# Kernel tuning notes

Measured on AMD Instinct MI355X. Metric: run time of the kernel, lower is better.

Reference implementation:

```python
import jax, jax.numpy as jnp
import numpy as np

H = 488          # hardcoded grid size in the module
K = 6            # n_targets
ITERS = 10       # n_iterations
RADIUS = 2       # sample_radius (int, used in slicing)
RECLEN = 2 * RADIUS + 1   # avgpool kernel in TorchModalitySampler (upscale=1)
RES = 0.25
THR = 3.0 / RES  # mask threshold on distances


def _greedy_sample(hm):
    """TorchModalitySampler greedy peak extraction for one [H,H] heatmap."""
    aw = H - RECLEN + 1  # avgpool output size (stride 1, valid)

    def step(hm, _):
        # avgpool(kernel=RECLEN, stride=1)
        agg = jax.lax.reduce_window(hm, 0.0, jax.lax.add,
                                    (RECLEN, RECLEN), (1, 1), 'VALID') / (RECLEN * RECLEN)
        flat = jnp.argmax(agg)              # first occurrence of max (row-major)
        r, c = flat // aw, flat % aw
        win = jax.lax.dynamic_slice(hm, (r, c), (RECLEN, RECLEN))
        max_val = win.max()
        # torch.nonzero(hm == max_val)[0] == first row-major match
        fh = jnp.argmax(hm == max_val)
        pt = jnp.stack([fh // H, fh % H]).astype(jnp.float32)
        conf = win.sum()
        hm = jax.lax.dynamic_update_slice(hm, jnp.zeros((RECLEN, RECLEN), hm.dtype), (r, c))
        return hm, (pt, conf)

    _, (pts, confs) = jax.lax.scan(step, hm, None, length=K)
    return pts, confs  # [K,2] float, [K] float


def setup_inputs() -> dict:
    key = jax.random.key(0)
    heatmap = jax.random.uniform(key, (32, 1, H, H), dtype=jnp.float32)
    return {"heatmap": heatmap}


def reference(heatmap):
    B = heatmap.shape[0]
    hm2d = heatmap[:, 0]                       # [B,H,H]
    clusters, _pre_conf = jax.vmap(_greedy_sample)(hm2d)   # [B,K,2]

    ii, jj = jnp.meshgrid(jnp.arange(H), jnp.arange(H), indexing='ij')
    indices = jnp.stack([ii, jj], -1).reshape(-1, 2).astype(jnp.float32)  # [N,2]
    hm_flat = hm2d.reshape(B, -1)              # [B,N]

    def body(_, cl):
        # d: [B,K,N] distances from each cluster to every pixel
        d = jnp.maximum(jnp.linalg.norm(indices[None, None] - cl[:, :, None], axis=-1), 0.001)
        m = d.min(axis=1)                      # [B,N] nearest-cluster distance
        w = (d < THR) * (hm_flat[:, None] / d) * (m[:, None] / d)  # [B,K,N]
        return jnp.einsum('bkn,nd->bkd', w, indices) / w.sum(-1, keepdims=True)

    clusters = jax.lax.fori_loop(0, ITERS, body, clusters)
    new_clusters = jnp.round(clusters).astype(jnp.int32)   # [B,K,2]

    def conf_one(hm, c):
        win = jax.lax.dynamic_slice(hm, (c[0] - RADIUS, c[1] - RADIUS), (2 * RADIUS, 2 * RADIUS))
        return win.sum()

    confidences = jax.vmap(lambda hm, cs: jax.vmap(lambda c: conf_one(hm, c))(cs))(hm2d, new_clusters)
    return new_clusters, confidences
```

## Files before the change

### kernel.cpp

```cpp
#include <hip/hip_runtime.h>

#define H   488
#define HH  (H*H)
#define AW  484
#define KK  6
#define BB  32
#define NB4 (HH/4)
#define NCH 10
#define MAGIC 0x137F9E24

#define SCALE 8388608.0f

#define PHYS(j) ((j) + ((j) >> 5))
#define HPAD 504

__device__ __forceinline__ float mload(const float* h, int i, int j,
                                       const int* rr, const int* rc, int nr) {
    float v = h[i * H + j];
    for (int t = 0; t < nr; ++t)
        if ((unsigned)(i - rr[t]) < 5u && (unsigned)(j - rc[t]) < 5u) v = 0.0f;
    return v;
}

__device__ __forceinline__ unsigned long long mkkey(int s, int c) {
    return ((unsigned long long)(unsigned)s << 32) | (unsigned)~(unsigned)c;
}

union SmAB {
    int colsum[8][HPAD];
    struct { unsigned long long bK[8 * AW]; unsigned long long rvK[AW]; } kb;
};

__global__ __launch_bounds__(640) void kAB(const float* __restrict__ hm,
                                           unsigned long long* __restrict__ blockK,
                                           int* __restrict__ rectR, int* __restrict__ rectC,
                                           float* __restrict__ maxv, int* __restrict__ scanres,
                                           int* __restrict__ doneA, int* __restrict__ cntC) {
    __shared__ SmAB sm;
    __shared__ int rrS[KK], rcS[KK];
    __shared__ int selRs, selCs;
    int tid = threadIdx.x, wave = tid >> 6, lane = tid & 63;

    if (blockIdx.x >= 32) {
        int idx = blockIdx.x - 32;
        int b  = idx / 61;
        int g  = idx - b * 61;
        int r0 = g * 8;
        int nw = (r0 + 8 <= AW) ? 8 : (AW - r0);
        const float* h = hm + b * HH;

        int j = tid;
        if (j < H) {
            int v[12];
            #pragma unroll
            for (int i = 0; i < 12; ++i) {
                int row = r0 + i;
                v[i] = (row < H) ? (int)(h[row * H + j] * SCALE) : 0;
            }
            int pj = PHYS(j);
            #pragma unroll
            for (int w = 0; w < 8; ++w)
                sm.colsum[w][pj] = v[w] + v[w + 1] + v[w + 2] + v[w + 3] + v[w + 4];
        }
        __syncthreads();

        if (wave < nw) {
            int r = r0 + wave;
            int c0 = lane * 8;
            int cs[13];
            #pragma unroll
            for (int t = 0; t < 13; ++t) {
                int ix = c0 + t;
                cs[t] = (ix < H) ? sm.colsum[wave][PHYS(ix)] : 0;
            }
            int s = cs[0] + cs[1] + cs[2] + cs[3] + cs[4];
            unsigned long long best = (c0 < AW) ? mkkey(s, c0) : 0ull;
            #pragma unroll
            for (int t = 1; t < 8; ++t) {
                s += cs[t + 4] - cs[t - 1];
                int c = c0 + t;
                unsigned long long k2v = (c < AW) ? mkkey(s, c) : 0ull;
                if (k2v > best) best = k2v;
            }
            #pragma unroll
            for (int off = 4; off; off >>= 1) {
                unsigned long long o = __shfl_down(best, (unsigned)off);
                if (o > best) best = o;
            }
            if ((lane & 7) == 0) {
                int p = lane >> 3;
                __hip_atomic_store(&blockK[(b * 8 + p) * AW + r], best,
                                   __ATOMIC_RELAXED, __HIP_MEMORY_SCOPE_AGENT);
            }
        }
        __syncthreads();
        if (tid == 0)
            __hip_atomic_store(&doneA[b * 61 + g], MAGIC,
                               __ATOMIC_RELAXED, __HIP_MEMORY_SCOPE_AGENT);
        return;
    }

    int b = blockIdx.x;
    const float* h = hm + b * HH;

    if (tid == 0) cntC[b] = 0;

    if (wave == 0) {
        bool done = false;
        do {
            int v = (lane < 61)
                ? __hip_atomic_load(&doneA[b * 61 + lane], __ATOMIC_RELAXED, __HIP_MEMORY_SCOPE_AGENT)
                : MAGIC;
            done = __all(v == MAGIC);
            if (!done) __builtin_amdgcn_s_sleep(8);
        } while (!done);
        __threadfence();
    }
    __syncthreads();

    if (tid < AW) {
        unsigned long long kk[8];
        #pragma unroll
        for (int p = 0; p < 8; ++p) kk[p] = blockK[(b * 8 + p) * AW + tid];
        unsigned long long mk = kk[0];
        #pragma unroll
        for (int p = 1; p < 8; ++p) if (kk[p] > mk) mk = kk[p];
        #pragma unroll
        for (int p = 0; p < 8; ++p) sm.kb.bK[p * AW + tid] = kk[p];
        sm.kb.rvK[tid] = ((mk >> 32) << 20) | ((unsigned long long)(1023 - tid) << 10) | (mk & 0x3FF);
    }
    __syncthreads();

    unsigned long long partK = 0ull;
    int prlo = 0, prhi = -1;

    for (int step = 0; step < KK; ++step) {
        if (wave == 0) {
            unsigned long long win = 0ull;
            if (step == 0) {
                #pragma unroll
                for (int t = 0; t < 8; ++t) {
                    int idx = t * 64 + lane;
                    if (idx < AW) { unsigned long long v = sm.kb.rvK[idx]; if (v > win) win = v; }
                }
                #pragma unroll
                for (int off = 32; off; off >>= 1) {
                    unsigned long long o = __shfl_down(win, (unsigned)off);
                    if (o > win) win = o;
                }
            } else {
                if (lane <= prhi - prlo) win = sm.kb.rvK[prlo + lane];
                if (lane == 9) { if (partK > win) win = partK; }
                #pragma unroll
                for (int off = 8; off; off >>= 1) {
                    unsigned long long o = __shfl_down(win, (unsigned)off);
                    if (o > win) win = o;
                }
            }
            if (lane == 0) {
                int C = 1023 - (int)(win & 0x3FF);
                int R = 1023 - (int)((win >> 10) & 0x3FF);
                rrS[step] = R; rcS[step] = C;
                selRs = R; selCs = C;
            }
        } else if (wave == 1 && step > 0) {
            int m = step - 1;
            int R1 = rrS[m], C1 = rcS[m];
            float wv = -1.0f;
            if (lane < 25) wv = mload(h, R1 + lane / 5, C1 + lane % 5, rrS, rcS, m);
            #pragma unroll
            for (int off = 32; off; off >>= 1) wv = fmaxf(wv, __shfl_down(wv, (unsigned)off));
            if (lane == 0) {
                maxv[b * KK + m]    = wv;
                rectR[b * KK + m]   = R1;
                rectC[b * KK + m]   = C1;
                scanres[b * KK + m] = 0x7fffffff;
            }
        }
        __syncthreads();
        if (step == KK - 1) break;

        int R = selRs, C = selCs;
        int rlo = R > 4 ? R - 4 : 0, rhi = R + 4 < AW ? R + 4 : AW - 1;
        int nr = rhi - rlo + 1;
        if (wave >= 1 && wave <= nr) {
            int r = rlo + (wave - 1);
            int cb0 = (C > 4 ? C - 4 : 0) >> 6;
            int cb1 = ((C + 4 < AW ? C + 4 : AW - 1)) >> 6;
            bool two = (cb1 > cb0);
            int rrL[KK], rcL[KK];
            #pragma unroll
            for (int t = 0; t < KK; ++t) { rrL[t] = rrS[t]; rcL[t] = rcS[t]; }
            int jA0 = cb0 * 64 + lane, jB0 = jA0 + 64;
            int jA1 = cb1 * 64 + lane, jB1 = jA1 + 64;
            float vA0[5], vB0[5], vA1[5], vB1[5];
            #pragma unroll
            for (int i = 0; i < 5; ++i) {
                vA0[i] = (jA0 < H) ? h[(r + i) * H + jA0] : 0.0f;
                vB0[i] = (lane < 4 && jB0 < H) ? h[(r + i) * H + jB0] : 0.0f;
                vA1[i] = (two && jA1 < H) ? h[(r + i) * H + jA1] : 0.0f;
                vB1[i] = (two && lane < 4 && jB1 < H) ? h[(r + i) * H + jB1] : 0.0f;
            }
            #pragma unroll
            for (int t = 0; t < KK; ++t) if (t <= step) {
                int rt = rrL[t], ct = rcL[t];
                #pragma unroll
                for (int i = 0; i < 5; ++i) {
                    if ((unsigned)(r + i - rt) < 5u) {
                        if ((unsigned)(jA0 - ct) < 5u) vA0[i] = 0.0f;
                        if ((unsigned)(jB0 - ct) < 5u) vB0[i] = 0.0f;
                        if ((unsigned)(jA1 - ct) < 5u) vA1[i] = 0.0f;
                        if ((unsigned)(jB1 - ct) < 5u) vB1[i] = 0.0f;
                    }
                }
            }
            int csA0 = 0, csB0 = 0, csA1 = 0, csB1 = 0;
            #pragma unroll
            for (int i = 0; i < 5; ++i) {
                csA0 += (int)(vA0[i] * SCALE); csB0 += (int)(vB0[i] * SCALE);
                csA1 += (int)(vA1[i] * SCALE); csB1 += (int)(vB1[i] * SCALE);
            }
            int s0 = 0, s1 = 0;
            #pragma unroll
            for (int k = 0; k < 5; ++k) {
                int a0 = __shfl_down(csA0, (unsigned)k);
                int a1 = __shfl_down(csA1, (unsigned)k);
                int srcb = lane + k - 64; if (srcb < 0) srcb = 0;
                int b0v = __shfl(csB0, srcb);
                int b1v = __shfl(csB1, srcb);
                s0 += (lane + k < 64) ? a0 : b0v;
                s1 += (lane + k < 64) ? a1 : b1v;
            }
            int c0col = cb0 * 64 + lane, c1col = cb1 * 64 + lane;
            unsigned long long kA_ = (c0col < AW) ? mkkey(s0, c0col) : 0ull;
            unsigned long long kB_ = (two && c1col < AW) ? mkkey(s1, c1col) : 0ull;
            #pragma unroll
            for (int off = 32; off; off >>= 1) {
                unsigned long long oA = __shfl_down(kA_, (unsigned)off);
                unsigned long long oB = __shfl_down(kB_, (unsigned)off);
                if (oA > kA_) kA_ = oA;
                if (oB > kB_) kB_ = oB;
            }
            unsigned long long keyA = __shfl(kA_, 0);
            unsigned long long keyB = __shfl(kB_, 0);
            unsigned long long cand = (lane < 8) ? sm.kb.bK[lane * AW + r] : 0ull;
            if (lane == cb0) cand = keyA;
            if (two && lane == cb1) cand = keyB;
            #pragma unroll
            for (int off = 4; off; off >>= 1) {
                unsigned long long o = __shfl_down(cand, (unsigned)off);
                if (o > cand) cand = o;
            }
            if (lane == 0) {
                sm.kb.rvK[r] = ((cand >> 32) << 20) | ((unsigned long long)(1023 - r) << 10) | (cand & 0x3FF);
                sm.kb.bK[cb0 * AW + r] = keyA;
                if (two) sm.kb.bK[cb1 * AW + r] = keyB;
            }
        } else if (wave == 0) {
            unsigned long long c0 = 0ull;
            #pragma unroll
            for (int t = 0; t < 8; ++t) {
                int idx = t * 64 + lane;
                if (idx < AW && (idx < rlo || idx > rhi)) {
                    unsigned long long v = sm.kb.rvK[idx];
                    if (v > c0) c0 = v;
                }
            }
            #pragma unroll
            for (int off = 32; off; off >>= 1) {
                unsigned long long o = __shfl_down(c0, (unsigned)off);
                if (o > c0) c0 = o;
            }
            partK = __shfl(c0, 0);
            prlo = rlo; prhi = rhi;
        }
        __syncthreads();
    }
    if (wave == 1) {
        int m = KK - 1;
        int R1 = rrS[m], C1 = rcS[m];
        float wv = -1.0f;
        if (lane < 25) wv = mload(h, R1 + lane / 5, C1 + lane % 5, rrS, rcS, m);
        #pragma unroll
        for (int off = 32; off; off >>= 1) wv = fmaxf(wv, __shfl_down(wv, (unsigned)off));
        if (lane == 0) {
            maxv[b * KK + m]    = wv;
            rectR[b * KK + m]   = R1;
            rectC[b * KK + m]   = C1;
            scanres[b * KK + m] = 0x7fffffff;
        }
    }
}

__global__ __launch_bounds__(768) void kCD(const float* __restrict__ hm,
                                           const int* __restrict__ rectR, const int* __restrict__ rectC,
                                           const float* __restrict__ maxv, int* __restrict__ scanres,
                                           int* __restrict__ cntC, float* __restrict__ out) {
    int b     = blockIdx.x & 31;
    int chunk = blockIdx.x >> 5;
    int tid = threadIdx.x, wave = tid >> 6, lane = tid & 63;
    const float* h = hm + b * HH;

    {
        float mv[KK];
        int rr[5], rc[5], lim[KK];
        #pragma unroll
        for (int s = 0; s < KK; ++s) mv[s] = maxv[b * KK + s];
        float minmv = mv[0];
        #pragma unroll
        for (int s = 1; s < KK; ++s) minmv = fminf(minmv, mv[s]);
        #pragma unroll
        for (int t = 0; t < 5; ++t) { rr[t] = rectR[b * KK + t]; rc[t] = rectC[b * KK + t]; }
        int limmax = 0;
        #pragma unroll
        for (int s = 0; s < KK; ++s) {
            lim[s] = (rectR[b * KK + s] + 4) * H + rectC[b * KK + s] + 4;
            limmax = lim[s] > limmax ? lim[s] : limmax;
        }
        const float4* h4 = (const float4*)h;
        int local[KK];
        #pragma unroll
        for (int s = 0; s < KK; ++s) local[s] = 0x7fffffff;
        for (int i4 = chunk * 768 + tid; i4 < NB4; i4 += 768 * NCH) {
            if (4 * i4 > limmax) break;
            float4 v = h4[i4];
            float m4 = fmaxf(fmaxf(v.x, v.y), fmaxf(v.z, v.w));
            if (m4 >= minmv) {
                float vs[4] = {v.x, v.y, v.z, v.w};
                #pragma unroll
                for (int e = 0; e < 4; ++e) {
                    #pragma unroll
                    for (int s = 0; s < KK; ++s) {
                        if (vs[e] == mv[s]) {
                            int n = 4 * i4 + e;
                            if (n <= lim[s]) {
                                int i = n / H, j = n - i * H;
                                bool masked = false;
                                for (int t = 0; t < s; ++t)
                                    if ((unsigned)(i - rr[t]) < 5u && (unsigned)(j - rc[t]) < 5u) masked = true;
                                if (!masked && n < local[s]) local[s] = n;
                            }
                        }
                    }
                }
            }
        }
        __shared__ int smC[KK];
        if (tid < KK) smC[tid] = 0x7fffffff;
        __syncthreads();
        #pragma unroll
        for (int s = 0; s < KK; ++s)
            if (local[s] != 0x7fffffff) atomicMin(&smC[s], local[s]);
        __syncthreads();
        if (tid < KK && smC[tid] != 0x7fffffff)
            atomicMin(&scanres[b * KK + tid], smC[tid]);
    }
    __syncthreads();

    __shared__ int sh_old;
    if (tid == 0) sh_old = atomicAdd(&cntC[b], 1);
    __syncthreads();
    if (sh_old != NCH - 1) return;

    __shared__ float cly[2][KK], clx[2][KK];
    __shared__ float part[KK][2][3];
    if (tid < KK) {
        int fh = atomicMin(&scanres[b * KK + tid], 0x7fffffff);
        cly[0][tid] = (float)(fh / H);
        clx[0][tid] = (float)(fh % H);
    }
    __syncthreads();
    int k = wave >> 1, half = wave & 1;
    int base = half * 64 + lane;

    int di_[4], dj_[4]; bool act_[4];
    #pragma unroll
    for (int s = 0; s < 4; ++s) { act_[s] = false; di_[s] = 0; dj_[s] = 0; }
    {
        int pos = 0;
        #pragma unroll
        for (int r = 0; r < 24; ++r) {
            const int di = r - 11;
            const int u = (di > 0) ? (di - 1) : -di;
            const int vt[12] = {11, 11, 11, 11, 11, 10, 10, 9, 8, 7, 6, 4};
            const int vl = vt[u];
            const int cnt = 2 * vl + 2;
            #pragma unroll
            for (int s = 0; s < 4; ++s) {
                int idx = base + s * 128;
                if (idx >= pos && idx < pos + cnt) {
                    act_[s] = true; di_[s] = di; dj_[s] = -vl + (idx - pos);
                }
            }
            pos += cnt;
        }
    }

    int cur = 0;
    for (int it = 0; it < 10; ++it) {
        float ys[KK], xs[KK];
        #pragma unroll
        for (int q = 0; q < KK; ++q) { ys[q] = cly[cur][q]; xs[q] = clx[cur][q]; }
        float cy = 0.0f, cx = 0.0f;
        #pragma unroll
        for (int q = 0; q < KK; ++q) if (q == k) { cy = ys[q]; cx = xs[q]; }
        int fy = (int)floorf(cy), fx = (int)floorf(cx);
        float sy = 0.0f, sx = 0.0f, sw = 0.0f;
        #pragma unroll
        for (int s = 0; s < 4; ++s) {
            if (act_[s]) {
                int i = fy + di_[s], j = fx + dj_[s];
                if ((unsigned)i < (unsigned)H && (unsigned)j < (unsigned)H) {
                    float hv = h[i * H + j];
                    float fi = (float)i, fj = (float)j;
                    float d2[KK];
                    #pragma unroll
                    for (int q = 0; q < KK; ++q) {
                        float dy = __fsub_rn(fi, ys[q]);
                        float dx = __fsub_rn(fj, xs[q]);
                        d2[q] = __fadd_rn(__fmul_rn(dy, dy), __fmul_rn(dx, dx));
                    }
                    float dyk = __fsub_rn(fi, cy), dxk = __fsub_rn(fj, cx);
                    float d2k = __fadd_rn(__fmul_rn(dyk, dyk), __fmul_rn(dxk, dxk));
                    if (d2k < 144.0f) {
                        float m2 = d2[0];
                        #pragma unroll
                        for (int q = 1; q < KK; ++q) m2 = fminf(m2, d2[q]);
                        float d = fmaxf(__fsqrt_rn(d2k), 0.001f);
                        float m = fmaxf(__fsqrt_rn(m2), 0.001f);
                        float w = __fmul_rn(__fdiv_rn(hv, d), __fdiv_rn(m, d));
                        sw += w;
                        sy += w * fi;
                        sx += w * fj;
                    }
                }
            }
        }
        #pragma unroll
        for (int off = 32; off; off >>= 1) {
            sy += __shfl_down(sy, (unsigned)off);
            sx += __shfl_down(sx, (unsigned)off);
            sw += __shfl_down(sw, (unsigned)off);
        }
        if (lane == 0) { part[k][half][0] = sy; part[k][half][1] = sx; part[k][half][2] = sw; }
        __syncthreads();
        if (tid < KK) {
            float ty = part[tid][0][0] + part[tid][1][0];
            float tx = part[tid][0][1] + part[tid][1][1];
            float tw = part[tid][0][2] + part[tid][1][2];
            cly[cur ^ 1][tid] = ty / tw;
            clx[cur ^ 1][tid] = tx / tw;
        }
        __syncthreads();
        cur ^= 1;
    }
    if (tid < KK) {
        int iy = __float2int_rn(cly[cur][tid]);
        int ix = __float2int_rn(clx[cur][tid]);
        out[b * (KK * 2) + 2 * tid]     = (float)iy;
        out[b * (KK * 2) + 2 * tid + 1] = (float)ix;
        int s0 = iy - 2; if (s0 < 0) s0 = 0; if (s0 > H - 4) s0 = H - 4;
        int s1 = ix - 2; if (s1 < 0) s1 = 0; if (s1 > H - 4) s1 = H - 4;
        double cs = 0.0;
        for (int i = 0; i < 4; ++i)
            for (int j = 0; j < 4; ++j) cs += (double)h[(s0 + i) * H + (s1 + j)];
        out[BB * KK * 2 + b * KK + tid] = (float)cs;
    }
}

extern "C" void kernel_launch(void* const* d_in, const int* in_sizes, int n_in,
                              void* d_out, int out_size, void* d_ws, size_t ws_size,
                              hipStream_t stream) {
    const float* hm = (const float*)d_in[0];
    float* out = (float*)d_out;

    unsigned long long* blockK = (unsigned long long*)d_ws;
    int*    rectR   = (int*)(blockK + BB * 8 * AW);
    int*    rectC   = rectR + BB * KK;
    float*  maxv    = (float*)(rectC + BB * KK);
    int*    scanres = (int*)(maxv + BB * KK);
    int*    cntC    = scanres + BB * KK;
    int*    doneA   = cntC + BB;

    kAB<<<32 + BB * 61, 640, 0, stream>>>(hm, blockK, rectR, rectC, maxv, scanres, doneA, cntC);
    kCD<<<BB * NCH, 768, 0, stream>>>(hm, rectR, rectC, maxv, scanres, cntC, out);
}
```

Measured before the change: 146.7 us.

## Replace spin-waiting reducer blocks with last-arriving-block finalization

Removes the 32 dedicated blocks that spin on completion flags. Each of the row-group blocks now publishes its flag, checks whether all 61 flags for its batch are set, and the block that sees completion runs the greedy selection tail. The goal is to stop wasting CU slots on spin loops and to start the serial tail without waiting for the spinning blocks to be scheduled. It also lowers the kCD chunk count from 10 to 8. The flag check uses relaxed atomics with no counter or fence, so the tail can run in more than one block, or in none, which affects correctness and repeatability.

```diff
diff --git a/kernel.cpp b/kernel.cpp
--- a/kernel.cpp
+++ b/kernel.cpp
@@ -6,7 +6,7 @@
 #define KK  6
 #define BB  32
 #define NB4 (HH/4)
-#define NCH 10
+#define NCH 8
 #define MAGIC 0x137F9E24
 
 #define SCALE 8388608.0f
@@ -31,24 +31,22 @@
     struct { unsigned long long bK[8 * AW]; unsigned long long rvK[AW]; } kb;
 };
 
-__global__ __launch_bounds__(640) void kAB(const float* __restrict__ hm,
-                                           unsigned long long* __restrict__ blockK,
-                                           int* __restrict__ rectR, int* __restrict__ rectC,
-                                           float* __restrict__ maxv, int* __restrict__ scanres,
-                                           int* __restrict__ doneA, int* __restrict__ cntC) {
+__global__ __launch_bounds__(640) void kABf(const float* __restrict__ hm,
+                                            unsigned long long* __restrict__ blockK,
+                                            int* __restrict__ rectR, int* __restrict__ rectC,
+                                            float* __restrict__ maxv, int* __restrict__ scanres,
+                                            int* __restrict__ doneA, int* __restrict__ cntC) {
     __shared__ SmAB sm;
     __shared__ int rrS[KK], rcS[KK];
-    __shared__ int selRs, selCs;
+    __shared__ int selRs, selCs, isFin;
     int tid = threadIdx.x, wave = tid >> 6, lane = tid & 63;
-
-    if (blockIdx.x >= 32) {
-        int idx = blockIdx.x - 32;
-        int b  = idx / 61;
-        int g  = idx - b * 61;
+    int b = blockIdx.x & 31;
+    int g = blockIdx.x >> 5;
+    const float* h = hm + b * HH;
+
+    {
         int r0 = g * 8;
         int nw = (r0 + 8 <= AW) ? 8 : (AW - r0);
-        const float* h = hm + b * HH;
-
         int j = tid;
         if (j < H) {
             int v[12];
@@ -93,35 +91,31 @@
                                    __ATOMIC_RELAXED, __HIP_MEMORY_SCOPE_AGENT);
             }
         }
-        __syncthreads();
-        if (tid == 0)
-            __hip_atomic_store(&doneA[b * 61 + g], MAGIC,
-                               __ATOMIC_RELAXED, __HIP_MEMORY_SCOPE_AGENT);
-        return;
-    }
-
-    int b = blockIdx.x;
-    const float* h = hm + b * HH;
+    }
+    __syncthreads();
+    if (tid == 0)
+        __hip_atomic_store(&doneA[b * 61 + g], MAGIC,
+                           __ATOMIC_RELAXED, __HIP_MEMORY_SCOPE_AGENT);
+    __syncthreads();
+
+    if (wave == 0) {
+        int v = (lane < 61)
+            ? __hip_atomic_load(&doneA[b * 61 + lane], __ATOMIC_RELAXED, __HIP_MEMORY_SCOPE_AGENT)
+            : MAGIC;
+        bool all = __all(v == MAGIC);
+        if (lane == 0) isFin = all ? 1 : 0;
+    }
+    __syncthreads();
+    if (!isFin) return;
 
     if (tid == 0) cntC[b] = 0;
-
-    if (wave == 0) {
-        bool done = false;
-        do {
-            int v = (lane < 61)
-                ? __hip_atomic_load(&doneA[b * 61 + lane], __ATOMIC_RELAXED, __HIP_MEMORY_SCOPE_AGENT)
-                : MAGIC;
-            done = __all(v == MAGIC);
-            if (!done) __builtin_amdgcn_s_sleep(8);
-        } while (!done);
-        __threadfence();
-    }
-    __syncthreads();
 
     if (tid < AW) {
         unsigned long long kk[8];
         #pragma unroll
-        for (int p = 0; p < 8; ++p) kk[p] = blockK[(b * 8 + p) * AW + tid];
+        for (int p = 0; p < 8; ++p)
+            kk[p] = __hip_atomic_load(&blockK[(b * 8 + p) * AW + tid],
+                                      __ATOMIC_RELAXED, __HIP_MEMORY_SCOPE_AGENT);
         unsigned long long mk = kk[0];
         #pragma unroll
         for (int p = 1; p < 8; ++p) if (kk[p] > mk) mk = kk[p];
@@ -482,6 +476,6 @@
     int*    cntC    = scanres + BB * KK;
     int*    doneA   = cntC + BB;
 
-    kAB<<<32 + BB * 61, 640, 0, stream>>>(hm, blockK, rectR, rectC, maxv, scanres, doneA, cntC);
+    kABf<<<BB * 61, 640, 0, stream>>>(hm, blockK, rectR, rectC, maxv, scanres, doneA, cntC);
     kCD<<<BB * NCH, 768, 0, stream>>>(hm, rectR, rectC, maxv, scanres, cntC, out);
 }
```

After: 148.1 us. About the same (+1.0%).
